# Performance work log

Measured on AMD Instinct MI355X. Metric: run time of the kernel, lower is better.

## Reference

```python
import jax, jax.numpy as jnp
import numpy as np

B, C, T, S = 128, 64, 8192, 16

def setup_inputs() -> dict:
    key = jax.random.key(0)
    k1, k2, k3, k4 = jax.random.split(key, 4)
    x = jax.random.normal(k1, (B, C, T), dtype=jnp.float32)
    subj_idx = jax.random.randint(k2, (B,), 0, S)
    # per-subject 1x1 conv == per-subject [C, C] matrix + bias.
    # (original identity-inits; we use identity + small noise so the op is non-trivial)
    W = jnp.eye(C, dtype=jnp.float32)[None] + 0.02 * jax.random.normal(k3, (S, C, C), dtype=jnp.float32)
    b = 0.02 * jax.random.normal(k4, (S, C), dtype=jnp.float32)
    return {"x": x, "subj_idx": subj_idx, "W": W, "b": b}

def reference(x, subj_idx, W, b):
    # Hard routing: gather each sample's subject weight, then batched 1x1 conv.
    Wb = W[subj_idx]            # [B, C_out, C_in]
    bb = b[subj_idx]            # [B, C_out]
    # out[b, o, t] = sum_c Wb[b, o, c] * x[b, c, t] + bb[b, o]
    return jnp.einsum('boc,bct->bot', Wb, x) + bb[:, :, None]
```

## Files before the change

### kernel.cpp

```cpp
#include <hip/hip_runtime.h>
#include <hip/hip_bf16.h>


typedef __attribute__((ext_vector_type(8))) short  bf16x8;
typedef __attribute__((ext_vector_type(16))) float f32x16;

namespace {
constexpr int Cdim  = 64;
constexpr int Tdim  = 8192;
constexpr int NSTEP = 16;
constexpr int BLOCK = 256;
}

static __device__ __forceinline__ short f2bf(float f) {
    return (short)__builtin_bit_cast(unsigned short, __float2bfloat16(f));
}

__global__ __launch_bounds__(BLOCK, 2)
void subject_layers_mfma32(const float* __restrict__ x,
                           const int*   __restrict__ subj,
                           const float* __restrict__ W,
                           const float* __restrict__ bias,
                           float*       __restrict__ out) {
    const int b    = blockIdx.y;
    const int tid  = threadIdx.x;
    const int wave = tid >> 6;
    const int lane = tid & 63;
    const int hi   = lane >> 5;
    const int ln   = lane & 31;
    const int s    = subj[b];

    const int t0 = (blockIdx.x * 4 + wave) * (NSTEP * 32);

    bf16x8 afrag[2][4];
    const float* Wb = W + (size_t)s * Cdim * Cdim;
    #pragma unroll
    for (int ot = 0; ot < 2; ++ot) {
        #pragma unroll
        for (int kb = 0; kb < 4; ++kb) {
            const float* ap = Wb + (size_t)(ot * 32 + ln) * Cdim + kb * 16 + hi * 8;
            const float4 a0 = *reinterpret_cast<const float4*>(ap);
            const float4 a1 = *reinterpret_cast<const float4*>(ap + 4);
            bf16x8 f;
            f[0] = f2bf(a0.x); f[1] = f2bf(a0.y); f[2] = f2bf(a0.z); f[3] = f2bf(a0.w);
            f[4] = f2bf(a1.x); f[5] = f2bf(a1.y); f[6] = f2bf(a1.z); f[7] = f2bf(a1.w);
            afrag[ot][kb] = f;
        }
    }

    f32x16 bini[2];
    const float* bb = bias + (size_t)s * Cdim;
    #pragma unroll
    for (int ot = 0; ot < 2; ++ot)
        #pragma unroll
        for (int r = 0; r < 16; ++r)
            bini[ot][r] = bb[ot * 32 + (r & 3) + 8 * (r >> 2) + 4 * hi];

    const float* xb = x   + (size_t)b * Cdim * Tdim + (size_t)(hi * 8) * Tdim + t0 + ln;
    float*       ob = out + (size_t)b * Cdim * Tdim + (size_t)(hi * 4) * Tdim + t0 + ln;

    float xr[4][8];
    #pragma unroll
    for (int kb = 0; kb < 4; ++kb)
        #pragma unroll
        for (int j = 0; j < 8; ++j)
            xr[kb][j] = xb[(size_t)(kb * 16 + j) * Tdim];

    #pragma unroll 4
    for (int step = 0; step < NSTEP; ++step) {
        float xn[4][8];
        if (step + 1 < NSTEP) {
            #pragma unroll
            for (int kb = 0; kb < 4; ++kb)
                #pragma unroll
                for (int j = 0; j < 8; ++j)
                    xn[kb][j] = xb[(size_t)(kb * 16 + j) * Tdim + (step + 1) * 32];
        }

        bf16x8 bfrag[4];
        #pragma unroll
        for (int kb = 0; kb < 4; ++kb) {
            bf16x8 f;
            #pragma unroll
            for (int j = 0; j < 8; ++j) f[j] = f2bf(xr[kb][j]);
            bfrag[kb] = f;
        }

        #pragma unroll
        for (int ot = 0; ot < 2; ++ot) {
            f32x16 acc = bini[ot];
            #pragma unroll
            for (int kb = 0; kb < 4; ++kb)
                acc = __builtin_amdgcn_mfma_f32_32x32x16_bf16(afrag[ot][kb], bfrag[kb], acc, 0, 0, 0);
            #pragma unroll
            for (int r = 0; r < 16; ++r)
                ob[(size_t)(ot * 32 + (r & 3) + 8 * (r >> 2)) * Tdim + step * 32] = acc[r];
        }

        #pragma unroll
        for (int kb = 0; kb < 4; ++kb)
            #pragma unroll
            for (int j = 0; j < 8; ++j)
                xr[kb][j] = xn[kb][j];
    }
}

extern "C" void kernel_launch(void* const* d_in, const int* in_sizes, int n_in,
                              void* d_out, int out_size, void* d_ws, size_t ws_size,
                              hipStream_t stream) {
    const float* x    = (const float*)d_in[0];
    const int*   subj = (const int*)  d_in[1];
    const float* W    = (const float*)d_in[2];
    const float* bias = (const float*)d_in[3];
    float*       out  = (float*)d_out;

    const int B = in_sizes[1];
    dim3 grid(Tdim / (4 * NSTEP * 32), B);
    dim3 block(BLOCK);
    hipLaunchKernelGGL(subject_layers_mfma32, grid, block, 0, stream,
                       x, subj, W, bias, out);
}
```

Baseline: 119.8 us.

## Stage x tile through LDS with float4 coalesced loads and stores

```diff
diff --git a/kernel.cpp b/kernel.cpp
--- a/kernel.cpp
+++ b/kernel.cpp
@@ -8,7 +8,8 @@
 namespace {
 constexpr int Cdim  = 64;
 constexpr int Tdim  = 8192;
-constexpr int NSTEP = 16;
+constexpr int TT    = 256;
+constexpr int STR   = TT + 4;
 constexpr int BLOCK = 256;
 }
 
@@ -17,12 +18,15 @@
 }
 
 __global__ __launch_bounds__(BLOCK, 2)
-void subject_layers_mfma32(const float* __restrict__ x,
-                           const int*   __restrict__ subj,
-                           const float* __restrict__ W,
-                           const float* __restrict__ bias,
-                           float*       __restrict__ out) {
+void subject_layers_r6(const float* __restrict__ x,
+                       const int*   __restrict__ subj,
+                       const float* __restrict__ W,
+                       const float* __restrict__ bias,
+                       float*       __restrict__ out) {
+    __shared__ float tile[Cdim * STR];
+
     const int b    = blockIdx.y;
+    const int tb   = blockIdx.x;
     const int tid  = threadIdx.x;
     const int wave = tid >> 6;
     const int lane = tid & 63;
@@ -30,7 +34,24 @@
     const int ln   = lane & 31;
     const int s    = subj[b];
 
-    const int t0 = (blockIdx.x * 4 + wave) * (NSTEP * 32);
+    const size_t xbase = (size_t)b * Cdim * Tdim + (size_t)tb * TT;
+
+    {
+        float4 v[4];
+        #pragma unroll
+        for (int gg = 0; gg < 4; ++gg) {
+            #pragma unroll
+            for (int g = 0; g < 4; ++g) {
+                const int row = (gg * 4 + g) * 4 + wave;
+                v[g] = *reinterpret_cast<const float4*>(x + xbase + (size_t)row * Tdim + lane * 4);
+            }
+            #pragma unroll
+            for (int g = 0; g < 4; ++g) {
+                const int row = (gg * 4 + g) * 4 + wave;
+                *reinterpret_cast<float4*>(&tile[row * STR + lane * 4]) = v[g];
+            }
+        }
+    }
 
     bf16x8 afrag[2][4];
     const float* Wb = W + (size_t)s * Cdim * Cdim;
@@ -56,52 +77,46 @@
         for (int r = 0; r < 16; ++r)
             bini[ot][r] = bb[ot * 32 + (r & 3) + 8 * (r >> 2) + 4 * hi];
 
-    const float* xb = x   + (size_t)b * Cdim * Tdim + (size_t)(hi * 8) * Tdim + t0 + ln;
-    float*       ob = out + (size_t)b * Cdim * Tdim + (size_t)(hi * 4) * Tdim + t0 + ln;
+    __syncthreads();
 
-    float xr[4][8];
+    bf16x8 bfrag[2][4];
     #pragma unroll
-    for (int kb = 0; kb < 4; ++kb)
-        #pragma unroll
-        for (int j = 0; j < 8; ++j)
-            xr[kb][j] = xb[(size_t)(kb * 16 + j) * Tdim];
-
-    #pragma unroll 4
-    for (int step = 0; step < NSTEP; ++step) {
-        float xn[4][8];
-        if (step + 1 < NSTEP) {
-            #pragma unroll
-            for (int kb = 0; kb < 4; ++kb)
-                #pragma unroll
-                for (int j = 0; j < 8; ++j)
-                    xn[kb][j] = xb[(size_t)(kb * 16 + j) * Tdim + (step + 1) * 32];
-        }
-
-        bf16x8 bfrag[4];
+    for (int st = 0; st < 2; ++st) {
+        const int col = wave * 64 + st * 32 + ln;
         #pragma unroll
         for (int kb = 0; kb < 4; ++kb) {
             bf16x8 f;
             #pragma unroll
-            for (int j = 0; j < 8; ++j) f[j] = f2bf(xr[kb][j]);
-            bfrag[kb] = f;
+            for (int j = 0; j < 8; ++j)
+                f[j] = f2bf(tile[(kb * 16 + hi * 8 + j) * STR + col]);
+            bfrag[st][kb] = f;
         }
+    }
 
+    __syncthreads();
+
+    #pragma unroll
+    for (int st = 0; st < 2; ++st) {
+        const int col = wave * 64 + st * 32 + ln;
         #pragma unroll
         for (int ot = 0; ot < 2; ++ot) {
             f32x16 acc = bini[ot];
             #pragma unroll
             for (int kb = 0; kb < 4; ++kb)
-                acc = __builtin_amdgcn_mfma_f32_32x32x16_bf16(afrag[ot][kb], bfrag[kb], acc, 0, 0, 0);
+                acc = __builtin_amdgcn_mfma_f32_32x32x16_bf16(afrag[ot][kb], bfrag[st][kb], acc, 0, 0, 0);
             #pragma unroll
             for (int r = 0; r < 16; ++r)
-                ob[(size_t)(ot * 32 + (r & 3) + 8 * (r >> 2)) * Tdim + step * 32] = acc[r];
+                tile[(ot * 32 + (r & 3) + 8 * (r >> 2) + 4 * hi) * STR + col] = acc[r];
         }
+    }
 
-        #pragma unroll
-        for (int kb = 0; kb < 4; ++kb)
-            #pragma unroll
-            for (int j = 0; j < 8; ++j)
-                xr[kb][j] = xn[kb][j];
+    __syncthreads();
+
+    #pragma unroll
+    for (int g = 0; g < 16; ++g) {
+        const int row = g * 4 + wave;
+        const float4 v = *reinterpret_cast<const float4*>(&tile[row * STR + lane * 4]);
+        *reinterpret_cast<float4*>(out + xbase + (size_t)row * Tdim + lane * 4) = v;
     }
 }
 
@@ -115,8 +130,8 @@
     float*       out  = (float*)d_out;
 
     const int B = in_sizes[1];
-    dim3 grid(Tdim / (4 * NSTEP * 32), B);
+    dim3 grid(Tdim / TT, B);
     dim3 block(BLOCK);
-    hipLaunchKernelGGL(subject_layers_mfma32, grid, block, 0, stream,
+    hipLaunchKernelGGL(subject_layers_r6, grid, block, 0, stream,
                        x, subj, W, bias, out);
 }
```

After: 105.3 us. -12.1%, faster.
